# Performance work log

Measured on AMD Instinct MI355X. Metric: run time of the kernel, lower is better.

Reference implementation:

```python
import jax, jax.numpy as jnp
import numpy as np

HEADS = 16

def setup_inputs() -> dict:
    key = jax.random.key(0)
    k1, k2, k3 = jax.random.split(key, 3)
    B, S, D = 2, 2048, 1024
    return {
        "query": jax.random.normal(k1, (B, S, D), dtype=jnp.float32),
        "key": jax.random.normal(k2, (B, S, D), dtype=jnp.float32),
        "value": jax.random.normal(k3, (B, S, D), dtype=jnp.float32),
    }

def reference(query, key, value):
    B, S, D = query.shape
    H = HEADS
    dh = D // H
    # split(-1) into H equal chunks == reshape to (B, S, H, dh)
    q = query.reshape(B, S, H, dh)
    k = key.reshape(B, S, H, dh)
    v = value.reshape(B, S, H, dh)
    scale = 1.0 / jnp.sqrt(jnp.asarray(dh, dtype=query.dtype))
    scores = jnp.einsum('bqhd,bkhd->bhqk', q, k) * scale  # [B,H,S,S]
    probs = jax.nn.softmax(scores, axis=-1)
    out = jnp.einsum('bhqk,bkhd->bqhd', probs, v)  # [B,S,H,dh]
    return out.reshape(B, S, D)
```

## Files before the change

### kernel.cpp

```cpp
#include <hip/hip_runtime.h>
#include <stdint.h>


#define B_ 2
#define S_ 2048
#define D_ 1024
#define H_ 16
#define DH 64
#define M_TILE 64

typedef __bf16 bf16;
typedef __bf16 bf16x2 __attribute__((ext_vector_type(2)));
typedef __bf16 bf16x4 __attribute__((ext_vector_type(4)));
typedef __bf16 bf16x8 __attribute__((ext_vector_type(8)));
typedef float floatx4 __attribute__((ext_vector_type(4)));

#define KB_HEAD (S_ * DH * 2)
#define KB_TOTAL (B_ * H_ * KB_HEAD)
#define WS_NEEDED (2u * KB_TOTAL)

#define O_STRIDE 36
#define SMEM_MAIN (128 * O_STRIDE * 4 + 512)

__device__ __forceinline__ float fast_exp2(float x) {
#if __has_builtin(__builtin_amdgcn_exp2f)
  return __builtin_amdgcn_exp2f(x);
#else
  return exp2f(x);
#endif
}

__global__ __launch_bounds__(256)
void prep(const float* __restrict__ Kg, const float* __restrict__ Vg,
          unsigned char* __restrict__ ws) {
  const int bid = blockIdx.x;
  const int tid = threadIdx.x;
  if (bid < 512) {
    __shared__ __align__(16) bf16 VTsh[64][136];
    const int head_lin = bid & 31, ktile = bid >> 5;
    const int b = head_lin >> 4, h = head_lin & 15;
    const int kb = ktile * 128;
    const int vr0 = (tid >> 3) << 2;
    const int vf0 = (tid & 7) << 3;
    const float* Vbase = Vg + (size_t)(b * S_) * D_ + h * DH;
    float vals[4][8];
#pragma unroll
    for (int rr = 0; rr < 4; ++rr) {
      const float* vp = Vbase + (size_t)(kb + vr0 + rr) * D_ + vf0;
      float4 a = *(const float4*)vp;
      float4 c = *(const float4*)(vp + 4);
      vals[rr][0] = a.x; vals[rr][1] = a.y; vals[rr][2] = a.z; vals[rr][3] = a.w;
      vals[rr][4] = c.x; vals[rr][5] = c.y; vals[rr][6] = c.z; vals[rr][7] = c.w;
    }
    const int pbase = (vr0 & 96) + ((vr0 >> 2) & 3) * 8 + ((vr0 >> 4) & 1) * 4;
#pragma unroll
    for (int j = 0; j < 8; ++j) {
      bf16x4 y = {(bf16)vals[0][j], (bf16)vals[1][j], (bf16)vals[2][j], (bf16)vals[3][j]};
      *(bf16x4*)(&VTsh[vf0 + j][pbase]) = y;
    }
    __syncthreads();
    unsigned char* Vout = ws + KB_TOTAL + (size_t)head_lin * KB_HEAD;
#pragma unroll
    for (int j = 0; j < 4; ++j) {
      const int id = j * 256 + tid;
      const int c   = id & 63;
      const int sub = id >> 6;
      const int fg  = sub & 3;
      const int ckl = sub >> 2;
      const int col = c & 15, quad = c >> 4;
      bf16x8 v = *(const bf16x8*)(&VTsh[fg * 16 + col][ckl * 32 + quad * 8]);
      const int blk = (ktile * 4 + ckl) * 4 + fg;
      *(bf16x8*)(Vout + ((size_t)blk << 10) + c * 16) = v;
    }
  } else {
    const int cb = bid - 512;
#pragma unroll
    for (int i = 0; i < 2; ++i) {
      const int id  = cb * 512 + i * 256 + tid;
      const int c   = id & 63;
      const int blk = id >> 6;
      const int hf  = blk & 1;
      const int g16 = (blk >> 1) & 127;
      const int head_lin = blk >> 8;
      const int col = c & 15, quad = c >> 4;
      const int bb = head_lin >> 4, hh = head_lin & 15;
      const int s = g16 * 16 + col;
      const float* src = Kg + (size_t)(bb * S_ + s) * D_ + hh * DH + hf * 32 + quad * 8;
      float4 x0 = ((const float4*)src)[0];
      float4 x1 = ((const float4*)src)[1];
      bf16x8 y = {(bf16)x0.x, (bf16)x0.y, (bf16)x0.z, (bf16)x0.w,
                  (bf16)x1.x, (bf16)x1.y, (bf16)x1.z, (bf16)x1.w};
      *(bf16x8*)(ws + (size_t)id * 16) = y;
    }
  }
}

__global__ __launch_bounds__(256, 4)
void attn_fwd(const float* __restrict__ Qg, const unsigned char* __restrict__ Kb,
              const unsigned char* __restrict__ VT, float* __restrict__ Og) {
  __shared__ __align__(16) unsigned char smem[SMEM_MAIN];
  float* Osh = (float*)smem;
  float* Lsh = (float*)(smem + 128 * O_STRIDE * 4);

  const int tid  = threadIdx.x;
  const int lane = tid & 63;
  const int wave = tid >> 6;
  const int kw   = wave & 1;
  const int qw   = wave >> 1;
  const int col  = lane & 15;
  const int quad = lane >> 4;

  const int bid      = blockIdx.x;
  const int head_lin = bid & 31;
  const int qtile    = bid >> 5;
  const int b        = head_lin >> 4;
  const int h        = head_lin & 15;

  const unsigned char* Khead = Kb + (size_t)head_lin * KB_HEAD;
  const unsigned char* Vhead = VT + (size_t)head_lin * KB_HEAD;

  const float QSCALE = 0.125f * 1.44269504088896340736f;

  bf16x8 Qf[2][2];
#pragma unroll
  for (int qt = 0; qt < 2; ++qt) {
    const float* base = Qg + (size_t)(b * S_ + qtile * M_TILE + qw * 32 + qt * 16 + col) * D_
                        + h * DH + quad * 8;
#pragma unroll
    for (int ks = 0; ks < 2; ++ks) {
      float4 x0 = *(const float4*)(base + ks * 32);
      float4 x1 = *(const float4*)(base + ks * 32 + 4);
      bf16x8 f;
      f[0] = (bf16)(x0.x * QSCALE); f[1] = (bf16)(x0.y * QSCALE);
      f[2] = (bf16)(x0.z * QSCALE); f[3] = (bf16)(x0.w * QSCALE);
      f[4] = (bf16)(x1.x * QSCALE); f[5] = (bf16)(x1.y * QSCALE);
      f[6] = (bf16)(x1.z * QSCALE); f[7] = (bf16)(x1.w * QSCALE);
      Qf[qt][ks] = f;
    }
  }

  floatx4 accO[4][2];
  float l_lane[2] = {0.f, 0.f};
#pragma unroll
  for (int ft = 0; ft < 4; ++ft)
#pragma unroll
    for (int qt = 0; qt < 2; ++qt) accO[ft][qt] = (floatx4)0.f;

  const int lane16 = lane * 16;

#pragma unroll 1
  for (int it = 0; it < 32; ++it) {
    const int ck = (qtile + it) & 31;
    const unsigned char* kp = Khead + (((size_t)(kw * 64 + ck * 2) * 2) << 10) + lane16;
    const unsigned char* vp = Vhead + (((size_t)(kw * 32 + ck) * 4) << 10) + lane16;

    bf16x8 Ka[2][2];
    Ka[0][0] = *(const bf16x8*)(kp);
    Ka[0][1] = *(const bf16x8*)(kp + 1024);
    Ka[1][0] = *(const bf16x8*)(kp + 2048);
    Ka[1][1] = *(const bf16x8*)(kp + 3072);
    bf16x8 Va[4];
    Va[0] = *(const bf16x8*)(vp);
    Va[1] = *(const bf16x8*)(vp + 1024);
    Va[2] = *(const bf16x8*)(vp + 2048);
    Va[3] = *(const bf16x8*)(vp + 3072);

    floatx4 accS[2][2];
#pragma unroll
    for (int kt = 0; kt < 2; ++kt)
#pragma unroll
      for (int qt = 0; qt < 2; ++qt) {
        floatx4 a = (floatx4)0.f;
        a = __builtin_amdgcn_mfma_f32_16x16x32_bf16(Ka[kt][0], Qf[qt][0], a, 0, 0, 0);
        a = __builtin_amdgcn_mfma_f32_16x16x32_bf16(Ka[kt][1], Qf[qt][1], a, 0, 0, 0);
        accS[kt][qt] = a;
      }

#pragma unroll
    for (int qt = 0; qt < 2; ++qt) {
      float rs = 0.f;
#pragma unroll
      for (int kt = 0; kt < 2; ++kt)
#pragma unroll
        for (int r = 0; r < 4; ++r) {
          float p = fast_exp2(accS[kt][qt][r]);
          accS[kt][qt][r] = p;
          rs += p;
        }
      l_lane[qt] += rs;
    }

    bf16x8 Pf[2];
#pragma unroll
    for (int qt = 0; qt < 2; ++qt) {
      floatx4 p0 = accS[0][qt], p1 = accS[1][qt];
      bf16x8 f = {(bf16)p0[0], (bf16)p0[1], (bf16)p0[2], (bf16)p0[3],
                  (bf16)p1[0], (bf16)p1[1], (bf16)p1[2], (bf16)p1[3]};
      Pf[qt] = f;
    }
#pragma unroll
    for (int ft = 0; ft < 4; ++ft)
#pragma unroll
      for (int qt = 0; qt < 2; ++qt)
        accO[ft][qt] = __builtin_amdgcn_mfma_f32_16x16x32_bf16(Va[ft], Pf[qt], accO[ft][qt], 0, 0, 0);
  }

  float l_red[2];
#pragma unroll
  for (int qt = 0; qt < 2; ++qt) {
    float s = l_lane[qt];
    s += __shfl_xor(s, 16);
    s += __shfl_xor(s, 32);
    l_red[qt] = s;
  }

  if (kw == 1) {
    float* r = Osh + (qw * 64 + lane) * O_STRIDE;
#pragma unroll
    for (int qt = 0; qt < 2; ++qt)
#pragma unroll
      for (int ft = 0; ft < 4; ++ft)
        *(floatx4*)(r + (qt * 4 + ft) * 4) = accO[ft][qt];
    if (quad == 0) {
#pragma unroll
      for (int qt = 0; qt < 2; ++qt)
        Lsh[qw * 32 + qt * 16 + col] = l_red[qt];
    }
  }
  __syncthreads();

  if (kw == 0) {
    const float* r = Osh + (qw * 64 + lane) * O_STRIDE;
    float rl[2];
#pragma unroll
    for (int qt = 0; qt < 2; ++qt)
      rl[qt] = 1.0f / (l_red[qt] + Lsh[qw * 32 + qt * 16 + col]);
#pragma unroll
    for (int qt = 0; qt < 2; ++qt) {
      const int q = qtile * M_TILE + qw * 32 + qt * 16 + col;
      float* dst = Og + (size_t)(b * S_ + q) * D_ + h * DH + quad * 4;
#pragma unroll
      for (int ft = 0; ft < 4; ++ft) {
        floatx4 o = (accO[ft][qt] + *(const floatx4*)(r + (qt * 4 + ft) * 4)) * rl[qt];
        *(floatx4*)(dst + ft * 16) = o;
      }
    }
  }
}

#define FB_NITER 16
#define FB_K_STRIDE 68
#define FB_V_STRIDE 132
#define FB_K_BYTES (128 * FB_K_STRIDE * 2)
#define FB_V_BYTES (64 * FB_V_STRIDE * 2)
#define FB_SMEM ((256 * O_STRIDE * 4 + 2048) > (FB_K_BYTES + FB_V_BYTES) ? (256 * O_STRIDE * 4 + 2048) : (FB_K_BYTES + FB_V_BYTES))

__device__ __forceinline__ bf16x8 cat8(bf16x4 a, bf16x4 b) {
  return __builtin_shufflevector(a, b, 0, 1, 2, 3, 4, 5, 6, 7);
}

__global__ __launch_bounds__(512, 4)
void attn_fwd_fb(const float* __restrict__ Qg, const float* __restrict__ Kg,
                 const float* __restrict__ Vg, float* __restrict__ Og) {
  __shared__ __align__(16) unsigned char smem[FB_SMEM];
  bf16*  Ksh = (bf16*)smem;
  bf16*  Vsh = (bf16*)(smem + FB_K_BYTES);
  float* Osh = (float*)smem;
  float* Lsh = (float*)(smem + 256 * O_STRIDE * 4);

  const int tid  = threadIdx.x;
  const int lane = tid & 63;
  const int wave = tid >> 6;
  const int kw   = wave & 1;
  const int qw   = wave >> 1;
  const int col  = lane & 15;
  const int quad = lane >> 4;
  const int bid      = blockIdx.x;
  const int head_lin = bid & 31;
  const int qtile    = bid >> 5;
  const int b        = head_lin >> 4;
  const int h        = head_lin & 15;
  const float QSCALE = 0.125f * 1.44269504088896340736f;

  bf16x8 Qf[2][2];
#pragma unroll
  for (int qt = 0; qt < 2; ++qt) {
    const float* base = Qg + (size_t)(b * S_ + qtile * 128 + qw * 32 + qt * 16 + col) * D_
                        + h * DH + quad * 8;
#pragma unroll
    for (int ks = 0; ks < 2; ++ks) {
      float4 x0 = *(const float4*)(base + ks * 32);
      float4 x1 = *(const float4*)(base + ks * 32 + 4);
      bf16x8 f;
      f[0] = (bf16)(x0.x * QSCALE); f[1] = (bf16)(x0.y * QSCALE);
      f[2] = (bf16)(x0.z * QSCALE); f[3] = (bf16)(x0.w * QSCALE);
      f[4] = (bf16)(x1.x * QSCALE); f[5] = (bf16)(x1.y * QSCALE);
      f[6] = (bf16)(x1.z * QSCALE); f[7] = (bf16)(x1.w * QSCALE);
      Qf[qt][ks] = f;
    }
  }

  floatx4 accO[4][2];
  float l_lane[2] = {0.f, 0.f};
#pragma unroll
  for (int ft = 0; ft < 4; ++ft)
#pragma unroll
    for (int qt = 0; qt < 2; ++qt) accO[ft][qt] = (floatx4)0.f;

  const float* Kbase = Kg + (size_t)(b * S_) * D_ + h * DH;
  const float* Vbase = Vg + (size_t)(b * S_) * D_ + h * DH;
  const int krow0 = tid >> 4;
  const int kf4   = tid & 15;
  const int vk0   = (tid >> 3) * 2;
  const int vf0   = (tid & 7) * 8;

  for (int it = 0; it < FB_NITER; ++it) {
    const int kb = it * 128;
    float4 kx[4];
#pragma unroll
    for (int i = 0; i < 4; ++i)
      kx[i] = *(const float4*)(Kbase + (size_t)(kb + krow0 + 32 * i) * D_ + kf4 * 4);
    float4 va0 = *(const float4*)(Vbase + (size_t)(kb + vk0) * D_ + vf0);
    float4 va1 = *(const float4*)(Vbase + (size_t)(kb + vk0) * D_ + vf0 + 4);
    float4 vb0 = *(const float4*)(Vbase + (size_t)(kb + vk0 + 1) * D_ + vf0);
    float4 vb1 = *(const float4*)(Vbase + (size_t)(kb + vk0 + 1) * D_ + vf0 + 4);
#pragma unroll
    for (int i = 0; i < 4; ++i) {
      bf16x4 y = {(bf16)kx[i].x, (bf16)kx[i].y, (bf16)kx[i].z, (bf16)kx[i].w};
      *(bf16x4*)(Ksh + (krow0 + 32 * i) * FB_K_STRIDE + kf4 * 4) = y;
    }
    {
      float a[8] = {va0.x, va0.y, va0.z, va0.w, va1.x, va1.y, va1.z, va1.w};
      float c[8] = {vb0.x, vb0.y, vb0.z, vb0.w, vb1.x, vb1.y, vb1.z, vb1.w};
#pragma unroll
      for (int j = 0; j < 8; ++j) {
        bf16x2 y = {(bf16)a[j], (bf16)c[j]};
        *(bf16x2*)(Vsh + (vf0 + j) * FB_V_STRIDE + vk0) = y;
      }
    }
    __syncthreads();

    floatx4 accS[4][2];
#pragma unroll
    for (int kt = 0; kt < 4; ++kt) {
      const bf16* kp = Ksh + (kw * 64 + kt * 16 + col) * FB_K_STRIDE + quad * 8;
      bf16x8 Ka0 = cat8(*(const bf16x4*)kp, *(const bf16x4*)(kp + 4));
      bf16x8 Ka1 = cat8(*(const bf16x4*)(kp + 32), *(const bf16x4*)(kp + 36));
#pragma unroll
      for (int qt = 0; qt < 2; ++qt) {
        floatx4 a = (floatx4)0.f;
        a = __builtin_amdgcn_mfma_f32_16x16x32_bf16(Ka0, Qf[qt][0], a, 0, 0, 0);
        a = __builtin_amdgcn_mfma_f32_16x16x32_bf16(Ka1, Qf[qt][1], a, 0, 0, 0);
        accS[kt][qt] = a;
      }
    }
#pragma unroll
    for (int qt = 0; qt < 2; ++qt) {
      float rs = 0.f;
#pragma unroll
      for (int kt = 0; kt < 4; ++kt)
#pragma unroll
        for (int r = 0; r < 4; ++r) {
          float p = fast_exp2(accS[kt][qt][r]);
          accS[kt][qt][r] = p;
          rs += p;
        }
      l_lane[qt] += rs;
    }
#pragma unroll
    for (int c = 0; c < 2; ++c) {
      bf16x8 Pf[2];
#pragma unroll
      for (int qt = 0; qt < 2; ++qt) {
        floatx4 p0 = accS[2 * c][qt], p1 = accS[2 * c + 1][qt];
        bf16x8 f = {(bf16)p0[0], (bf16)p0[1], (bf16)p0[2], (bf16)p0[3],
                    (bf16)p1[0], (bf16)p1[1], (bf16)p1[2], (bf16)p1[3]};
        Pf[qt] = f;
      }
#pragma unroll
      for (int ft = 0; ft < 4; ++ft) {
        const bf16* vp = Vsh + (ft * 16 + col) * FB_V_STRIDE + kw * 64 + 32 * c + quad * 4;
        bf16x8 Va = cat8(*(const bf16x4*)vp, *(const bf16x4*)(vp + 16));
#pragma unroll
        for (int qt = 0; qt < 2; ++qt)
          accO[ft][qt] = __builtin_amdgcn_mfma_f32_16x16x32_bf16(Va, Pf[qt], accO[ft][qt], 0, 0, 0);
      }
    }
    __syncthreads();
  }

  float l_red[2];
#pragma unroll
  for (int qt = 0; qt < 2; ++qt) {
    float s = l_lane[qt];
    s += __shfl_xor(s, 16);
    s += __shfl_xor(s, 32);
    l_red[qt] = s;
  }
  if (kw == 1) {
    float* r = Osh + (qw * 64 + lane) * O_STRIDE;
#pragma unroll
    for (int qt = 0; qt < 2; ++qt)
#pragma unroll
      for (int ft = 0; ft < 4; ++ft)
        *(floatx4*)(r + (qt * 4 + ft) * 4) = accO[ft][qt];
    if (quad == 0) {
#pragma unroll
      for (int qt = 0; qt < 2; ++qt)
        Lsh[qw * 32 + qt * 16 + col] = l_red[qt];
    }
  }
  __syncthreads();
  if (kw == 0) {
    const float* r = Osh + (qw * 64 + lane) * O_STRIDE;
    float rl[2];
#pragma unroll
    for (int qt = 0; qt < 2; ++qt)
      rl[qt] = 1.0f / (l_red[qt] + Lsh[qw * 32 + qt * 16 + col]);
#pragma unroll
    for (int qt = 0; qt < 2; ++qt) {
      const int q = qtile * 128 + qw * 32 + qt * 16 + col;
      float* dst = Og + (size_t)(b * S_ + q) * D_ + h * DH + quad * 4;
#pragma unroll
      for (int ft = 0; ft < 4; ++ft) {
        floatx4 o = (accO[ft][qt] + *(const floatx4*)(r + (qt * 4 + ft) * 4)) * rl[qt];
        *(floatx4*)(dst + ft * 16) = o;
      }
    }
  }
}

extern "C" void kernel_launch(void* const* d_in, const int* in_sizes, int n_in,
                              void* d_out, int out_size, void* d_ws, size_t ws_size,
                              hipStream_t stream) {
  const float* Q = (const float*)d_in[0];
  const float* K = (const float*)d_in[1];
  const float* V = (const float*)d_in[2];
  float* O = (float*)d_out;
  if (ws_size >= WS_NEEDED && d_ws != nullptr) {
    unsigned char* ws = (unsigned char*)d_ws;
    hipLaunchKernelGGL(prep, dim3(1536), dim3(256), 0, stream, K, V, ws);
    hipLaunchKernelGGL(attn_fwd, dim3(B_ * H_ * (S_ / M_TILE)), dim3(256), 0, stream,
                       Q, ws, ws + KB_TOTAL, O);
  } else {
    hipLaunchKernelGGL(attn_fwd_fb, dim3(512), dim3(512), 0, stream, Q, K, V, O);
  }
}
```

Baseline: 132.4 us.

## Split keys four ways per block with each wave covering all 64 queries

Restructures the main attention kernel so each of the four waves handles all 64 query rows over a quarter of the key range, instead of a 2x2 split of query and key halves. Each K/V fragment loaded from global memory now feeds four query tiles rather than two, which halves K/V traffic per block. In exchange the cross-wave reduction of partial outputs grows: three waves write partials to shared memory in four column chunks, with eight barriers, and wave 0 sums them. Register pressure rises, so launch bounds drop from 4 to 2 blocks per SIMD.

```diff
diff --git a/kernel.cpp b/kernel.cpp
--- a/kernel.cpp
+++ b/kernel.cpp
@@ -19,8 +19,9 @@
 #define KB_TOTAL (B_ * H_ * KB_HEAD)
 #define WS_NEEDED (2u * KB_TOTAL)
 
-#define O_STRIDE 36
-#define SMEM_MAIN (128 * O_STRIDE * 4 + 512)
+#define MR_STRIDE 20
+#define MR_BYTES (3 * 64 * MR_STRIDE * 4)
+#define SMEM_MAIN (MR_BYTES + 1024)
 
 __device__ __forceinline__ float fast_exp2(float x) {
 #if __has_builtin(__builtin_amdgcn_exp2f)
@@ -95,18 +96,16 @@
   }
 }
 
-__global__ __launch_bounds__(256, 4)
+__global__ __launch_bounds__(256, 2)
 void attn_fwd(const float* __restrict__ Qg, const unsigned char* __restrict__ Kb,
               const unsigned char* __restrict__ VT, float* __restrict__ Og) {
   __shared__ __align__(16) unsigned char smem[SMEM_MAIN];
   float* Osh = (float*)smem;
-  float* Lsh = (float*)(smem + 128 * O_STRIDE * 4);
+  float* Lsh = (float*)(smem + MR_BYTES);
 
   const int tid  = threadIdx.x;
   const int lane = tid & 63;
-  const int wave = tid >> 6;
-  const int kw   = wave & 1;
-  const int qw   = wave >> 1;
+  const int kw   = tid >> 6;
   const int col  = lane & 15;
   const int quad = lane >> 4;
 
@@ -121,10 +120,10 @@
 
   const float QSCALE = 0.125f * 1.44269504088896340736f;
 
-  bf16x8 Qf[2][2];
-#pragma unroll
-  for (int qt = 0; qt < 2; ++qt) {
-    const float* base = Qg + (size_t)(b * S_ + qtile * M_TILE + qw * 32 + qt * 16 + col) * D_
+  bf16x8 Qf[4][2];
+#pragma unroll
+  for (int qt = 0; qt < 4; ++qt) {
+    const float* base = Qg + (size_t)(b * S_ + qtile * M_TILE + qt * 16 + col) * D_
                         + h * DH + quad * 8;
 #pragma unroll
     for (int ks = 0; ks < 2; ++ks) {
@@ -139,20 +138,20 @@
     }
   }
 
-  floatx4 accO[4][2];
-  float l_lane[2] = {0.f, 0.f};
+  floatx4 accO[4][4];
+  float l_lane[4] = {0.f, 0.f, 0.f, 0.f};
 #pragma unroll
   for (int ft = 0; ft < 4; ++ft)
 #pragma unroll
-    for (int qt = 0; qt < 2; ++qt) accO[ft][qt] = (floatx4)0.f;
+    for (int qt = 0; qt < 4; ++qt) accO[ft][qt] = (floatx4)0.f;
 
   const int lane16 = lane * 16;
 
 #pragma unroll 1
-  for (int it = 0; it < 32; ++it) {
-    const int ck = (qtile + it) & 31;
-    const unsigned char* kp = Khead + (((size_t)(kw * 64 + ck * 2) * 2) << 10) + lane16;
-    const unsigned char* vp = Vhead + (((size_t)(kw * 32 + ck) * 4) << 10) + lane16;
+  for (int it = 0; it < 16; ++it) {
+    const int c = kw * 16 + ((qtile + it) & 15);
+    const unsigned char* kp = Khead + (((size_t)c * 4) << 10) + lane16;
+    const unsigned char* vp = Vhead + (((size_t)c * 4) << 10) + lane16;
 
     bf16x8 Ka[2][2];
     Ka[0][0] = *(const bf16x8*)(kp);
@@ -165,11 +164,11 @@
     Va[2] = *(const bf16x8*)(vp + 2048);
     Va[3] = *(const bf16x8*)(vp + 3072);
 
-    floatx4 accS[2][2];
+    floatx4 accS[2][4];
 #pragma unroll
     for (int kt = 0; kt < 2; ++kt)
 #pragma unroll
-      for (int qt = 0; qt < 2; ++qt) {
+      for (int qt = 0; qt < 4; ++qt) {
         floatx4 a = (floatx4)0.f;
         a = __builtin_amdgcn_mfma_f32_16x16x32_bf16(Ka[kt][0], Qf[qt][0], a, 0, 0, 0);
         a = __builtin_amdgcn_mfma_f32_16x16x32_bf16(Ka[kt][1], Qf[qt][1], a, 0, 0, 0);
@@ -177,7 +176,7 @@
       }
 
 #pragma unroll
-    for (int qt = 0; qt < 2; ++qt) {
+    for (int qt = 0; qt < 4; ++qt) {
       float rs = 0.f;
 #pragma unroll
       for (int kt = 0; kt < 2; ++kt)
@@ -190,61 +189,67 @@
       l_lane[qt] += rs;
     }
 
-    bf16x8 Pf[2];
-#pragma unroll
-    for (int qt = 0; qt < 2; ++qt) {
+#pragma unroll
+    for (int qt = 0; qt < 4; ++qt) {
       floatx4 p0 = accS[0][qt], p1 = accS[1][qt];
-      bf16x8 f = {(bf16)p0[0], (bf16)p0[1], (bf16)p0[2], (bf16)p0[3],
-                  (bf16)p1[0], (bf16)p1[1], (bf16)p1[2], (bf16)p1[3]};
-      Pf[qt] = f;
-    }
-#pragma unroll
-    for (int ft = 0; ft < 4; ++ft)
-#pragma unroll
-      for (int qt = 0; qt < 2; ++qt)
-        accO[ft][qt] = __builtin_amdgcn_mfma_f32_16x16x32_bf16(Va[ft], Pf[qt], accO[ft][qt], 0, 0, 0);
-  }
-
-  float l_red[2];
-#pragma unroll
-  for (int qt = 0; qt < 2; ++qt) {
+      bf16x8 Pf = {(bf16)p0[0], (bf16)p0[1], (bf16)p0[2], (bf16)p0[3],
+                   (bf16)p1[0], (bf16)p1[1], (bf16)p1[2], (bf16)p1[3]};
+#pragma unroll
+      for (int ft = 0; ft < 4; ++ft)
+        accO[ft][qt] = __builtin_amdgcn_mfma_f32_16x16x32_bf16(Va[ft], Pf, accO[ft][qt], 0, 0, 0);
+    }
+  }
+
+  float l_red[4];
+#pragma unroll
+  for (int qt = 0; qt < 4; ++qt) {
     float s = l_lane[qt];
     s += __shfl_xor(s, 16);
     s += __shfl_xor(s, 32);
     l_red[qt] = s;
   }
 
-  if (kw == 1) {
-    float* r = Osh + (qw * 64 + lane) * O_STRIDE;
-#pragma unroll
-    for (int qt = 0; qt < 2; ++qt)
-#pragma unroll
-      for (int ft = 0; ft < 4; ++ft)
-        *(floatx4*)(r + (qt * 4 + ft) * 4) = accO[ft][qt];
+  if (kw != 0) {
     if (quad == 0) {
 #pragma unroll
-      for (int qt = 0; qt < 2; ++qt)
-        Lsh[qw * 32 + qt * 16 + col] = l_red[qt];
-    }
-  }
-  __syncthreads();
-
-  if (kw == 0) {
-    const float* r = Osh + (qw * 64 + lane) * O_STRIDE;
-    float rl[2];
-#pragma unroll
-    for (int qt = 0; qt < 2; ++qt)
-      rl[qt] = 1.0f / (l_red[qt] + Lsh[qw * 32 + qt * 16 + col]);
-#pragma unroll
-    for (int qt = 0; qt < 2; ++qt) {
-      const int q = qtile * M_TILE + qw * 32 + qt * 16 + col;
-      float* dst = Og + (size_t)(b * S_ + q) * D_ + h * DH + quad * 4;
-#pragma unroll
-      for (int ft = 0; ft < 4; ++ft) {
-        floatx4 o = (accO[ft][qt] + *(const floatx4*)(r + (qt * 4 + ft) * 4)) * rl[qt];
-        *(floatx4*)(dst + ft * 16) = o;
-      }
-    }
+      for (int qt = 0; qt < 4; ++qt)
+        Lsh[(kw - 1) * 64 + qt * 16 + col] = l_red[qt];
+    }
+  }
+
+  float rl[4];
+#pragma unroll
+  for (int c = 0; c < 4; ++c) {
+    if (kw != 0) {
+      float* r = Osh + ((kw - 1) * 64) * MR_STRIDE;
+#pragma unroll
+      for (int qt = 0; qt < 4; ++qt)
+        *(floatx4*)(r + (qt * 16 + col) * MR_STRIDE + quad * 4) = accO[c][qt];
+    }
+    __syncthreads();
+
+    if (c == 0 && kw == 0) {
+#pragma unroll
+      for (int qt = 0; qt < 4; ++qt) {
+        const int q = qt * 16 + col;
+        rl[qt] = 1.0f / (l_red[qt] + Lsh[q] + Lsh[64 + q] + Lsh[128 + q]);
+      }
+    }
+
+    if (kw == 0) {
+#pragma unroll
+      for (int qt = 0; qt < 4; ++qt) {
+        const int q = qt * 16 + col;
+        floatx4 acc = accO[c][qt];
+#pragma unroll
+        for (int w = 0; w < 3; ++w)
+          acc += *(const floatx4*)(Osh + (w * 64 + q) * MR_STRIDE + quad * 4);
+        float* dst = Og + (size_t)(b * S_ + qtile * M_TILE + q) * D_ + h * DH
+                     + c * 16 + quad * 4;
+        *(floatx4*)dst = acc * rl[qt];
+      }
+    }
+    __syncthreads();
   }
 }
 
@@ -253,7 +258,8 @@
 #define FB_V_STRIDE 132
 #define FB_K_BYTES (128 * FB_K_STRIDE * 2)
 #define FB_V_BYTES (64 * FB_V_STRIDE * 2)
-#define FB_SMEM ((256 * O_STRIDE * 4 + 2048) > (FB_K_BYTES + FB_V_BYTES) ? (256 * O_STRIDE * 4 + 2048) : (FB_K_BYTES + FB_V_BYTES))
+#define FB_O_STRIDE 36
+#define FB_SMEM ((256 * FB_O_STRIDE * 4 + 2048) > (FB_K_BYTES + FB_V_BYTES) ? (256 * FB_O_STRIDE * 4 + 2048) : (FB_K_BYTES + FB_V_BYTES))
 
 __device__ __forceinline__ bf16x8 cat8(bf16x4 a, bf16x4 b) {
   return __builtin_shufflevector(a, b, 0, 1, 2, 3, 4, 5, 6, 7);
@@ -266,7 +272,7 @@
   bf16*  Ksh = (bf16*)smem;
   bf16*  Vsh = (bf16*)(smem + FB_K_BYTES);
   float* Osh = (float*)smem;
-  float* Lsh = (float*)(smem + 256 * O_STRIDE * 4);
+  float* Lsh = (float*)(smem + 256 * FB_O_STRIDE * 4);
 
   const int tid  = threadIdx.x;
   const int lane = tid & 63;
@@ -398,7 +404,7 @@
     l_red[qt] = s;
   }
   if (kw == 1) {
-    float* r = Osh + (qw * 64 + lane) * O_STRIDE;
+    float* r = Osh + (qw * 64 + lane) * FB_O_STRIDE;
 #pragma unroll
     for (int qt = 0; qt < 2; ++qt)
 #pragma unroll
@@ -412,7 +418,7 @@
   }
   __syncthreads();
   if (kw == 0) {
-    const float* r = Osh + (qw * 64 + lane) * O_STRIDE;
+    const float* r = Osh + (qw * 64 + lane) * FB_O_STRIDE;
     float rl[2];
 #pragma unroll
     for (int qt = 0; qt < 2; ++qt)
```

Result: no change. 133.7 us (+1.0%).
